# Kernel optimization log

Hardware: AMD Instinct MI355X
Metric: run time of the kernel (lower is better)

## Reference

```python
import jax, jax.numpy as jnp
import numpy as np

B, N, C = 8, 1024, 768
H = 12
HD = C // H
FF = 2048
NUM_CLASSES = 1000
SCALE = HD ** -0.5


def layer_norm(x, g, b, eps=1e-5):
    mu = jnp.mean(x, axis=-1, keepdims=True)
    var = jnp.var(x, axis=-1, keepdims=True)
    return (x - mu) * jax.lax.rsqrt(var + eps) * g + b


def setup_inputs() -> dict:
    key = jax.random.key(0)
    ks = jax.random.split(key, 12)
    s = lambda *sh: 0.02
    return {
        "src": jax.random.normal(ks[0], (B, N, C), jnp.float32),
        "y": jax.random.uniform(ks[1], (B, NUM_CLASSES), jnp.float32),
        "scorenet_h_src": jax.random.normal(ks[2], (B, NUM_CLASSES), jnp.float32),
        "pre_g": jnp.ones((C,), jnp.float32),
        "pre_b": jnp.zeros((C,), jnp.float32),
        "qkv_w": jax.random.normal(ks[3], (C, 3 * C), jnp.float32) * 0.02,
        "proj_w": jax.random.normal(ks[4], (C, C), jnp.float32) * 0.02,
        "proj_b": jnp.zeros((C,), jnp.float32),
        "n1_g": jnp.ones((C,), jnp.float32),
        "n1_b": jnp.zeros((C,), jnp.float32),
        "l1_w": jax.random.normal(ks[5], (C, FF), jnp.float32) * 0.02,
        "l1_b": jnp.zeros((FF,), jnp.float32),
        "l2_w": jax.random.normal(ks[6], (FF, C), jnp.float32) * 0.02,
        "l2_b": jnp.zeros((C,), jnp.float32),
    }


def attention(x, qkv_w, proj_w, proj_b):
    # x: [B, N, C] -> qkv: [B, N, 3, H, HD]
    qkv = (x @ qkv_w).reshape(B, N, 3, H, HD)
    qkv = jnp.transpose(qkv, (2, 0, 3, 1, 4))  # [3, B, H, N, HD]
    q, k, v = qkv[0], qkv[1], qkv[2]
    attn = jax.nn.softmax(jnp.einsum("bhqd,bhkd->bhqk", q, k) * SCALE, axis=-1)
    out = jnp.einsum("bhqk,bhkd->bhqd", attn, v)  # [B, H, N, HD]
    out = jnp.transpose(out, (0, 2, 1, 3)).reshape(B, N, C)
    out = out @ proj_w + proj_b
    return out, attn


def reference(src, y, scorenet_h_src, pre_g, pre_b, qkv_w, proj_w, proj_b,
              n1_g, n1_b, l1_w, l1_b, l2_w, l2_b):
    # eval-mode forward: dropout / drop_path are identity, mixup branches off
    x, attn = attention(layer_norm(src, pre_g, pre_b), qkv_w, proj_w, proj_b)
    src = src + x
    src_n = layer_norm(src, n1_g, n1_b)
    ffn = jax.nn.gelu(src_n @ l1_w + l1_b, approximate=False) @ l2_w + l2_b
    src = src_n + ffn
    return (src, scorenet_h_src, y, attn)
```

## Files before the change

### kernel.cpp

```cpp
#include <hip/hip_runtime.h>
#include <stdint.h>

typedef unsigned short u16;
typedef __bf16 bf16x8 __attribute__((ext_vector_type(8)));
typedef float f32x4 __attribute__((ext_vector_type(4)));


__device__ __forceinline__ u16 f2bf(float f) {
  union { float f; unsigned u; } v; v.f = f;
  unsigned r = v.u + 0x7fffu + ((v.u >> 16) & 1u);
  return (u16)(r >> 16);
}
__device__ __forceinline__ float bf2f(unsigned u) {
  union { unsigned u; float f; } v; v.u = u << 16; return v.f;
}

__device__ __forceinline__ void async16(const void* g, void* l) {
  __builtin_amdgcn_global_load_lds(
      (const __attribute__((address_space(1))) void*)g,
      (__attribute__((address_space(3))) void*)l, 16, 0, 0);
}

__device__ __forceinline__ f32x4 mfma16(bf16x8 a, bf16x8 b, f32x4 c) {
  return __builtin_amdgcn_mfma_f32_16x16x32_bf16(a, b, c, 0, 0, 0);
}

__device__ __forceinline__ float gelu_exact(float x) {
  return 0.5f * x * (1.0f + erff(x * 0.70710678118654752440f));
}

#define VMCNT(n) asm volatile("s_waitcnt vmcnt(" #n ")" ::: "memory")
#define LGKM0 asm volatile("s_waitcnt lgkmcnt(0)" ::: "memory")
#define SCHED0 __builtin_amdgcn_sched_barrier(0)
#define BAR __builtin_amdgcn_s_barrier()

__global__ __launch_bounds__(256) void ln_kernel(
    const float* __restrict__ x, const float* __restrict__ g,
    const float* __restrict__ b, u16* __restrict__ obf,
    float* __restrict__ of) {
  const size_t row = blockIdx.x;
  const float* xr = x + row * 768;
  const int t = threadIdx.x;
  const int w = t >> 6, lane = t & 63;
  float v0 = xr[t], v1 = xr[t + 256], v2 = xr[t + 512];
  float s = v0 + v1 + v2;
  float sq = v0 * v0 + v1 * v1 + v2 * v2;
#pragma unroll
  for (int off = 32; off > 0; off >>= 1) {
    s += __shfl_down(s, off);
    sq += __shfl_down(sq, off);
  }
  __shared__ float ss[4], ssq[4];
  if (lane == 0) { ss[w] = s; ssq[w] = sq; }
  __syncthreads();
  s = ss[0] + ss[1] + ss[2] + ss[3];
  sq = ssq[0] + ssq[1] + ssq[2] + ssq[3];
  const float mean = s * (1.0f / 768.0f);
  const float var = sq * (1.0f / 768.0f) - mean * mean;
  const float rstd = rsqrtf(var + 1e-5f);
  float y0 = (v0 - mean) * rstd * g[t] + b[t];
  float y1 = (v1 - mean) * rstd * g[t + 256] + b[t + 256];
  float y2 = (v2 - mean) * rstd * g[t + 512] + b[t + 512];
  obf[row * 768 + t] = f2bf(y0);
  obf[row * 768 + t + 256] = f2bf(y1);
  obf[row * 768 + t + 512] = f2bf(y2);
  if (of) {
    of[row * 768 + t] = y0;
    of[row * 768 + t + 256] = y1;
    of[row * 768 + t + 512] = y2;
  }
}

__device__ __forceinline__ void transpose_tile(float (*tile)[33],
                                               const float* __restrict__ W,
                                               u16* __restrict__ Wt, int K,
                                               int N, int bx, int by) {
  const int n0 = bx * 32, k0 = by * 32;
  const int tx = threadIdx.x, ty = threadIdx.y;
  for (int r = ty; r < 32; r += 8)
    tile[r][tx] = W[(size_t)(k0 + r) * N + n0 + tx];
  __syncthreads();
  for (int r = ty; r < 32; r += 8)
    Wt[(size_t)(n0 + r) * K + k0 + tx] = f2bf(tile[tx][r]);
}

__global__ void misc_kernel(const float* __restrict__ qkv_w,
                            const float* __restrict__ proj_w,
                            const float* __restrict__ l1_w,
                            const float* __restrict__ l2_w,
                            u16* __restrict__ qkvwT, u16* __restrict__ projwT,
                            u16* __restrict__ l1wT, u16* __restrict__ l2wT,
                            const float* __restrict__ y,
                            const float* __restrict__ sc,
                            float* __restrict__ out) {
  __shared__ float tile[32][33];
  int bid = blockIdx.x;
  if (bid < 1728) { transpose_tile(tile, qkv_w, qkvwT, 768, 2304, bid % 72, bid / 72); return; }
  bid -= 1728;
  if (bid < 576) { transpose_tile(tile, proj_w, projwT, 768, 768, bid % 24, bid / 24); return; }
  bid -= 576;
  if (bid < 1536) { transpose_tile(tile, l1_w, l1wT, 768, 2048, bid % 64, bid / 64); return; }
  bid -= 1536;
  if (bid < 1536) { transpose_tile(tile, l2_w, l2wT, 2048, 768, bid % 24, bid / 24); return; }
  bid -= 1536;
  const int t = threadIdx.y * 32 + threadIdx.x;
  const int i = bid * 256 + t;
  if (i < 8000) {
    out[6291456 + i] = sc[i];
    out[6299456 + i] = y[i];
  }
}

__global__ void vt_kernel(const u16* __restrict__ qkv, u16* __restrict__ vt) {
  const int bh = blockIdx.z, b = bh / 12, h = bh % 12;
  const int n0 = blockIdx.x * 32, d0 = blockIdx.y * 32;
  __shared__ u16 tile[32][33];
  const u16* Vp = qkv + (size_t)b * 1024 * 2304 + 1536 + h * 64;
  const int tx = threadIdx.x, ty = threadIdx.y;
  for (int r = ty; r < 32; r += 8)
    tile[r][tx] = Vp[(size_t)(n0 + r) * 2304 + d0 + tx];
  __syncthreads();
  u16* Op = vt + (size_t)bh * 64 * 1024;
  for (int r = ty; r < 32; r += 8)
    Op[(size_t)(d0 + r) * 1024 + n0 + tx] = tile[tx][r];
}

template <int BM, int BN, int GN, int WM, int WN>
__global__ __launch_bounds__(256) void gemm_kernel(
    const u16* __restrict__ A, int lda, const u16* __restrict__ Bt, int ldb,
    const float* __restrict__ bias, const float* __restrict__ res,
    float* __restrict__ outF, u16* __restrict__ outB, int ldc, int K,
    int act) {
  __shared__ u16 As[2][BM * 32];
  __shared__ u16 Bs[2][BN * 32];
  const int tid = threadIdx.x;
  const int w = tid >> 6, lane = tid & 63;
  const size_t mBase = (size_t)blockIdx.y * BM;
  const size_t nBase = (size_t)blockIdx.x * BN;
  const int rq = lane >> 2;
  const int k8 = (lane & 3) * 8;
  const int wmBase = (w / GN) * (WM * 16);
  const int wnBase = (w % GN) * (WN * 16);
  const int tm = lane & 15, kq = lane >> 4;
  const f32x4 zero = {0.f, 0.f, 0.f, 0.f};
  f32x4 acc[WM][WN];
#pragma unroll
  for (int i = 0; i < WM; i++)
#pragma unroll
    for (int j = 0; j < WN; j++) acc[i][j] = zero;

#pragma unroll
  for (int c = w; c < BM / 16; c += 4)
    async16(A + (mBase + c * 16 + rq) * lda + k8, &As[0][c * 16 * 32]);
#pragma unroll
  for (int c = w; c < BN / 16; c += 4)
    async16(Bt + (nBase + c * 16 + rq) * ldb + k8, &Bs[0][c * 16 * 32]);

  int cur = 0;
  for (int kt = 0; kt < K; kt += 32) {
    __syncthreads();
    if (kt + 32 < K) {
      const int nxt = cur ^ 1;
#pragma unroll
      for (int c = w; c < BM / 16; c += 4)
        async16(A + (mBase + c * 16 + rq) * lda + kt + 32 + k8,
                &As[nxt][c * 16 * 32]);
#pragma unroll
      for (int c = w; c < BN / 16; c += 4)
        async16(Bt + (nBase + c * 16 + rq) * ldb + kt + 32 + k8,
                &Bs[nxt][c * 16 * 32]);
    }
    bf16x8 af[WM], bfv[WN];
#pragma unroll
    for (int i = 0; i < WM; i++)
      af[i] = *(const bf16x8*)&As[cur][(wmBase + i * 16 + tm) * 32 + kq * 8];
#pragma unroll
    for (int j = 0; j < WN; j++)
      bfv[j] = *(const bf16x8*)&Bs[cur][(wnBase + j * 16 + tm) * 32 + kq * 8];
#pragma unroll
    for (int i = 0; i < WM; i++)
#pragma unroll
      for (int j = 0; j < WN; j++) acc[i][j] = mfma16(af[i], bfv[j], acc[i][j]);
    cur ^= 1;
  }

#pragma unroll
  for (int i = 0; i < WM; i++) {
    const size_t row0 = mBase + wmBase + i * 16 + kq * 4;
#pragma unroll
    for (int j = 0; j < WN; j++) {
      const size_t col = nBase + wnBase + j * 16 + tm;
      const float bv = bias ? bias[col] : 0.0f;
#pragma unroll
      for (int r = 0; r < 4; r++) {
        const size_t rr = row0 + r;
        float v = acc[i][j][r] + bv;
        if (act) v = gelu_exact(v);
        if (res) v += res[rr * ldc + col];
        if (outF) outF[rr * ldc + col] = v;
        if (outB) outB[rr * ldc + col] = f2bf(v);
      }
    }
  }
}

#define QUAD(P)                                                              \
  __builtin_amdgcn_s_setprio(1);                                             \
  _Pragma("unroll") for (int i2 = 0; i2 < 2; ++i2) {                         \
    _Pragma("unroll") for (int j = 0; j < 4; ++j) {                          \
      acc[(P)*2 + i2][j] = mfma16(aF[i2][0], bF[j][0], acc[(P)*2 + i2][j]);  \
      acc[(P)*2 + i2][j] = mfma16(aF[i2][1], bF[j][1], acc[(P)*2 + i2][j]);  \
    }                                                                        \
  }                                                                          \
  __builtin_amdgcn_s_setprio(0);

template <int ACT>
__global__ __launch_bounds__(512, 2) void gemm256_kernel(
    const u16* __restrict__ A, int lda, const u16* __restrict__ Bt, int ldb,
    const float* __restrict__ bias, u16* __restrict__ outB, int ldc, int K,
    int NX, int nwg8) {
  __shared__ u16 As[2][256 * 64];
  __shared__ u16 Bs[2][256 * 64];
  const int tid = threadIdx.x;
  const int w = tid >> 6, lane = tid & 63;
  const int wr = w >> 2, wc = w & 3;
  const int tm = lane & 15, kq = lane >> 4;
  const int id = blockIdx.x;
  const int wg = (id & 7) * nwg8 + (id >> 3);
  const size_t mBase = (size_t)(wg / NX) * 256;
  const size_t nBase = (size_t)(wg % NX) * 256;
  const int srow = tid >> 3;
  const int gch = (tid & 7) ^ (srow & 7);

#define STAGE_B(buf, kt, rb)                                          \
  async16(Bt + (nBase + (rb) + srow) * (size_t)ldb + (kt) + gch * 8,  \
          &Bs[buf][(rb) * 64 + tid * 8])
#define STAGE_A(buf, kt, rb)                                          \
  async16(A + (mBase + (rb) + srow) * (size_t)lda + (kt) + gch * 8,   \
          &As[buf][(rb) * 64 + tid * 8])

  f32x4 acc[8][4];
  const f32x4 zero = {0.f, 0.f, 0.f, 0.f};
#pragma unroll
  for (int i = 0; i < 8; ++i)
#pragma unroll
    for (int j = 0; j < 4; ++j) acc[i][j] = zero;

  auto rdA = [&](int buf, int i, int s) -> bf16x8 {
    const int rl = wr * 128 + i * 16 + tm;
    const int ch = (s * 4 + kq) ^ (rl & 7);
    return *(const bf16x8*)&As[buf][rl * 64 + ch * 8];
  };
  auto rdB = [&](int buf, int j, int s) -> bf16x8 {
    const int rl = wc * 64 + j * 16 + tm;
    const int ch = (s * 4 + kq) ^ (rl & 7);
    return *(const bf16x8*)&Bs[buf][rl * 64 + ch * 8];
  };

  STAGE_B(0, 0, 0); STAGE_B(0, 0, 64); STAGE_B(0, 0, 128); STAGE_B(0, 0, 192);
  STAGE_A(0, 0, 0); STAGE_A(0, 0, 128); STAGE_A(0, 0, 64); STAGE_A(0, 0, 192);
  VMCNT(2);
  BAR;

  const int T = K >> 6;
  bf16x8 bF[4][2], aF[2][2];
  for (int t = 0; t < T; ++t) {
    const int cur = t & 1, nxt = cur ^ 1;
    const int kt1 = (t + 1) << 6;
    const bool last = (t == T - 1);
#pragma unroll
    for (int j = 0; j < 4; ++j) { bF[j][0] = rdB(cur, j, 0); bF[j][1] = rdB(cur, j, 1); }
    aF[0][0] = rdA(cur, 0, 0); aF[0][1] = rdA(cur, 0, 1);
    aF[1][0] = rdA(cur, 1, 0); aF[1][1] = rdA(cur, 1, 1);
    if (!last) { STAGE_B(nxt, kt1, 0); STAGE_B(nxt, kt1, 64); }
    BAR; LGKM0; SCHED0;
    QUAD(0);
    BAR;
    aF[0][0] = rdA(cur, 2, 0); aF[0][1] = rdA(cur, 2, 1);
    aF[1][0] = rdA(cur, 3, 0); aF[1][1] = rdA(cur, 3, 1);
    if (!last) { STAGE_B(nxt, kt1, 128); STAGE_B(nxt, kt1, 192); VMCNT(4); }
    else { VMCNT(0); }
    BAR; LGKM0; SCHED0;
    QUAD(1);
    BAR;
    aF[0][0] = rdA(cur, 4, 0); aF[0][1] = rdA(cur, 4, 1);
    aF[1][0] = rdA(cur, 5, 0); aF[1][1] = rdA(cur, 5, 1);
    if (!last) { STAGE_A(nxt, kt1, 0); STAGE_A(nxt, kt1, 128); }
    BAR; LGKM0; SCHED0;
    QUAD(2);
    BAR;
    aF[0][0] = rdA(cur, 6, 0); aF[0][1] = rdA(cur, 6, 1);
    aF[1][0] = rdA(cur, 7, 0); aF[1][1] = rdA(cur, 7, 1);
    if (!last) { STAGE_A(nxt, kt1, 64); STAGE_A(nxt, kt1, 192); VMCNT(2); }
    BAR; LGKM0; SCHED0;
    QUAD(3);
    BAR;
  }

#pragma unroll
  for (int i = 0; i < 8; ++i) {
    const size_t row0 = mBase + wr * 128 + i * 16 + kq * 4;
#pragma unroll
    for (int j = 0; j < 4; ++j) {
      const size_t col = nBase + wc * 64 + j * 16 + tm;
      const float bv = bias ? bias[col] : 0.0f;
#pragma unroll
      for (int r = 0; r < 4; ++r) {
        float v = acc[i][j][r] + bv;
        if (ACT) v = gelu_exact(v);
        outB[(row0 + r) * ldc + col] = f2bf(v);
      }
    }
  }
#undef STAGE_A
#undef STAGE_B
}

__global__ __launch_bounds__(256, 3) void flash_kernel(
    const u16* __restrict__ qkv, const u16* __restrict__ vt,
    float* __restrict__ attn, u16* __restrict__ aout) {
  __shared__ u16 Qs[32 * 64];
  __shared__ u16 KV[2 * 128 * 64];
  __shared__ u16 Ps[32 * 128];
  __shared__ float psum[4][32];
  __shared__ float rinv[32];
  const int tid = threadIdx.x;
  const int w = tid >> 6, lane = tid & 63;
  const int tm = lane & 15, kq = lane >> 4;
  const int bh = blockIdx.y, b = bh / 12, h = bh % 12;
  const size_t m0 = (size_t)blockIdx.x * 32;
  const u16* Qp = qkv + (size_t)b * 1024 * 2304 + h * 64;
  const u16* Kp = Qp + 768;
  const u16* Vp = vt + (size_t)bh * 64 * 1024;
  float* Ab = attn + ((size_t)bh * 1024 + m0) * 1024;

  {
    const int r = tid >> 3, c = tid & 7;
    *(uint4*)&Qs[r * 64 + ((c ^ (r & 7)) * 8)] =
        *(const uint4*)(Qp + (m0 + r) * 2304 + c * 8);
  }
  __syncthreads();
  bf16x8 aq[2][2];
#pragma unroll
  for (int i = 0; i < 2; i++)
#pragma unroll
    for (int k2 = 0; k2 < 2; k2++) {
      const int m = i * 16 + tm;
      aq[i][k2] =
          *(const bf16x8*)&Qs[m * 64 + (((k2 * 4 + kq) ^ (m & 7)) * 8)];
    }

  f32x4 rs[2] = {{0.f, 0.f, 0.f, 0.f}, {0.f, 0.f, 0.f, 0.f}};
  for (int cc = 0; cc < 4; ++cc) {
    const int nc = cc * 256;
    __syncthreads();
#pragma unroll
    for (int u = 0; u < 8; ++u) {
      const int idx = u * 256 + tid;
      const int r = idx >> 3, c = idx & 7;
      *(uint4*)&KV[r * 64 + ((c ^ (r & 7)) * 8)] =
          *(const uint4*)(Kp + (size_t)(nc + r) * 2304 + c * 8);
    }
    __syncthreads();
#pragma unroll
    for (int jj = 0; jj < 4; ++jj) {
      const int n = (w * 4 + jj) * 16 + tm;
      bf16x8 bk[2];
#pragma unroll
      for (int k2 = 0; k2 < 2; k2++)
        bk[k2] =
            *(const bf16x8*)&KV[n * 64 + (((k2 * 4 + kq) ^ (n & 7)) * 8)];
#pragma unroll
      for (int i = 0; i < 2; i++) {
        f32x4 s = {0.f, 0.f, 0.f, 0.f};
        s = mfma16(aq[i][0], bk[0], s);
        s = mfma16(aq[i][1], bk[1], s);
#pragma unroll
        for (int r = 0; r < 4; r++) rs[i][r] += __expf(s[r] * 0.125f);
      }
    }
  }
#pragma unroll
  for (int i = 0; i < 2; i++)
#pragma unroll
    for (int r = 0; r < 4; r++) {
      float v = rs[i][r];
      v += __shfl_xor(v, 1); v += __shfl_xor(v, 2);
      v += __shfl_xor(v, 4); v += __shfl_xor(v, 8);
      if (tm == 0) psum[w][i * 16 + kq * 4 + r] = v;
    }
  __syncthreads();
  if (tid < 32)
    rinv[tid] =
        1.0f / (psum[0][tid] + psum[1][tid] + psum[2][tid] + psum[3][tid]);

  const f32x4 zero = {0.f, 0.f, 0.f, 0.f};
  f32x4 oacc[2] = {zero, zero};
  const int mi = w & 1, dp = w >> 1;
  for (int cc = 0; cc < 8; ++cc) {
    const int nc = cc * 128;
    __syncthreads();
#pragma unroll
    for (int u = 0; u < 4; ++u) {
      const int idx = u * 256 + tid;
      const int r = idx >> 3, c = idx & 7;
      *(uint4*)&KV[r * 64 + ((c ^ (r & 7)) * 8)] =
          *(const uint4*)(Kp + (size_t)(nc + r) * 2304 + c * 8);
    }
#pragma unroll
    for (int u = 0; u < 4; ++u) {
      const int idx = u * 256 + tid;
      const int d = idx >> 4, c = idx & 15;
      *(uint4*)&KV[8192 + d * 128 + ((c ^ (d & 15)) * 8)] =
          *(const uint4*)(Vp + (size_t)d * 1024 + nc + c * 8);
    }
    __syncthreads();
#pragma unroll
    for (int jj = 0; jj < 2; ++jj) {
      const int nb = w * 2 + jj;
      const int n = nb * 16 + tm;
      bf16x8 bk[2];
#pragma unroll
      for (int k2 = 0; k2 < 2; k2++)
        bk[k2] =
            *(const bf16x8*)&KV[n * 64 + (((k2 * 4 + kq) ^ (n & 7)) * 8)];
#pragma unroll
      for (int i = 0; i < 2; i++) {
        f32x4 s = {0.f, 0.f, 0.f, 0.f};
        s = mfma16(aq[i][0], bk[0], s);
        s = mfma16(aq[i][1], bk[1], s);
        const int row = i * 16 + kq * 4;
#pragma unroll
        for (int r = 0; r < 4; r++) {
          const float p = __expf(s[r] * 0.125f) * rinv[row + r];
          Ab[(size_t)(row + r) * 1024 + nc + nb * 16 + tm] = p;
          const int pr = row + r, pn = nb * 16 + tm;
          Ps[pr * 128 + (((pn >> 3) ^ (pr & 7)) * 8) + (pn & 7)] = f2bf(p);
        }
      }
    }
    __syncthreads();
#pragma unroll
    for (int k2 = 0; k2 < 4; ++k2) {
      const int m = mi * 16 + tm;
      const bf16x8 ap =
          *(const bf16x8*)&Ps[m * 128 + (((k2 * 4 + kq) ^ (m & 7)) * 8)];
#pragma unroll
      for (int jd = 0; jd < 2; ++jd) {
        const int d = dp * 32 + jd * 16 + tm;
        const bf16x8 bv = *(const bf16x8*)&KV[8192 + d * 128 +
                                              (((k2 * 4 + kq) ^ (d & 15)) * 8)];
        oacc[jd] = mfma16(ap, bv, oacc[jd]);
      }
    }
  }
#pragma unroll
  for (int jd = 0; jd < 2; ++jd)
#pragma unroll
    for (int r = 0; r < 4; ++r) {
      const size_t gm = (size_t)b * 1024 + m0 + mi * 16 + kq * 4 + r;
      aout[gm * 768 + h * 64 + dp * 32 + jd * 16 + tm] = f2bf(oacc[jd][r]);
    }
}

extern "C" void kernel_launch(void* const* d_in, const int* in_sizes, int n_in,
                              void* d_out, int out_size, void* d_ws,
                              size_t ws_size, hipStream_t stream) {
  const float* src    = (const float*)d_in[0];
  const float* yin    = (const float*)d_in[1];
  const float* scin   = (const float*)d_in[2];
  const float* pre_g  = (const float*)d_in[3];
  const float* pre_b  = (const float*)d_in[4];
  const float* qkv_w  = (const float*)d_in[5];
  const float* proj_w = (const float*)d_in[6];
  const float* proj_b = (const float*)d_in[7];
  const float* n1_g   = (const float*)d_in[8];
  const float* n1_b   = (const float*)d_in[9];
  const float* l1_w   = (const float*)d_in[10];
  const float* l1_b   = (const float*)d_in[11];
  const float* l2_w   = (const float*)d_in[12];
  const float* l2_b   = (const float*)d_in[13];
  float* outp = (float*)d_out;
  float* attn = outp + 6307456;

  char* ws = (char*)d_ws;
  u16* qkvwT  = (u16*)(ws + 0ull);
  u16* projwT = (u16*)(ws + 3538944ull);
  u16* l1wT   = (u16*)(ws + 4718592ull);
  u16* l2wT   = (u16*)(ws + 7864320ull);
  const size_t P0 = 11010048ull;
  u16* xn   = (u16*)(ws + P0);
  u16* qkv  = (u16*)(ws + P0 + 12582912ull);
  u16* vt   = (u16*)(ws + P0 + 50331648ull);
  u16* aout = (u16*)(ws + P0 + 62914560ull);
  float* src2 = (float*)(ws + P0);
  u16*  snb   = (u16*)(ws + P0 + 25165824ull);
  u16*  hbuf  = (u16*)(ws + P0 + 37748736ull);
  float* snf  = (float*)(ws + P0 + 71303168ull);

  dim3 tb(32, 8);
  misc_kernel<<<5439, tb, 0, stream>>>(qkv_w, proj_w, l1_w, l2_w, qkvwT,
                                       projwT, l1wT, l2wT, yin, scin, outp);
  ln_kernel<<<8192, 256, 0, stream>>>(src, pre_g, pre_b, xn, nullptr);
  gemm256_kernel<0><<<288, 512, 0, stream>>>(xn, 768, qkvwT, 768, nullptr,
                                             qkv, 2304, 768, 9, 36);
  vt_kernel<<<dim3(32, 2, 96), tb, 0, stream>>>(qkv, vt);
  flash_kernel<<<dim3(32, 96), 256, 0, stream>>>(qkv, vt, attn, aout);
  gemm_kernel<64, 128, 4, 4, 2><<<dim3(6, 128), 256, 0, stream>>>(
      aout, 768, projwT, 768, proj_b, src, src2, nullptr, 768, 768, 0);
  ln_kernel<<<8192, 256, 0, stream>>>(src2, n1_g, n1_b, snb, snf);
  gemm256_kernel<1><<<256, 512, 0, stream>>>(snb, 768, l1wT, 768, l1_b,
                                             hbuf, 2048, 768, 8, 32);
  gemm_kernel<64, 128, 4, 4, 2><<<dim3(6, 128), 256, 0, stream>>>(
      hbuf, 2048, l2wT, 2048, l2_b, snf, outp, nullptr, 768, 2048, 0);
}
```

Before: 807.1 us.

## Use 256x256 pipelined GEMM for proj/FFN2 and vectorize attention-prob stores

Replaces the simple 64x128 GEMM used for the projection and second FFN layer with the tuned 256x256 gemm256 kernel. That kernel gains residual-add and fp32-output epilogue support. In the flash kernel, each lane's four probability values are transposed across lanes with shuffles so the fp32 attention matrix is written with float4 stores instead of scalar stores. The larger tiles give only 96 workgroups for the two N=768 GEMMs, which can leave many CUs idle.

```diff
diff --git a/kernel.cpp b/kernel.cpp
--- a/kernel.cpp
+++ b/kernel.cpp
@@ -125,85 +125,6 @@
     Op[(size_t)(d0 + r) * 1024 + n0 + tx] = tile[tx][r];
 }
 
-template <int BM, int BN, int GN, int WM, int WN>
-__global__ __launch_bounds__(256) void gemm_kernel(
-    const u16* __restrict__ A, int lda, const u16* __restrict__ Bt, int ldb,
-    const float* __restrict__ bias, const float* __restrict__ res,
-    float* __restrict__ outF, u16* __restrict__ outB, int ldc, int K,
-    int act) {
-  __shared__ u16 As[2][BM * 32];
-  __shared__ u16 Bs[2][BN * 32];
-  const int tid = threadIdx.x;
-  const int w = tid >> 6, lane = tid & 63;
-  const size_t mBase = (size_t)blockIdx.y * BM;
-  const size_t nBase = (size_t)blockIdx.x * BN;
-  const int rq = lane >> 2;
-  const int k8 = (lane & 3) * 8;
-  const int wmBase = (w / GN) * (WM * 16);
-  const int wnBase = (w % GN) * (WN * 16);
-  const int tm = lane & 15, kq = lane >> 4;
-  const f32x4 zero = {0.f, 0.f, 0.f, 0.f};
-  f32x4 acc[WM][WN];
-#pragma unroll
-  for (int i = 0; i < WM; i++)
-#pragma unroll
-    for (int j = 0; j < WN; j++) acc[i][j] = zero;
-
-#pragma unroll
-  for (int c = w; c < BM / 16; c += 4)
-    async16(A + (mBase + c * 16 + rq) * lda + k8, &As[0][c * 16 * 32]);
-#pragma unroll
-  for (int c = w; c < BN / 16; c += 4)
-    async16(Bt + (nBase + c * 16 + rq) * ldb + k8, &Bs[0][c * 16 * 32]);
-
-  int cur = 0;
-  for (int kt = 0; kt < K; kt += 32) {
-    __syncthreads();
-    if (kt + 32 < K) {
-      const int nxt = cur ^ 1;
-#pragma unroll
-      for (int c = w; c < BM / 16; c += 4)
-        async16(A + (mBase + c * 16 + rq) * lda + kt + 32 + k8,
-                &As[nxt][c * 16 * 32]);
-#pragma unroll
-      for (int c = w; c < BN / 16; c += 4)
-        async16(Bt + (nBase + c * 16 + rq) * ldb + kt + 32 + k8,
-                &Bs[nxt][c * 16 * 32]);
-    }
-    bf16x8 af[WM], bfv[WN];
-#pragma unroll
-    for (int i = 0; i < WM; i++)
-      af[i] = *(const bf16x8*)&As[cur][(wmBase + i * 16 + tm) * 32 + kq * 8];
-#pragma unroll
-    for (int j = 0; j < WN; j++)
-      bfv[j] = *(const bf16x8*)&Bs[cur][(wnBase + j * 16 + tm) * 32 + kq * 8];
-#pragma unroll
-    for (int i = 0; i < WM; i++)
-#pragma unroll
-      for (int j = 0; j < WN; j++) acc[i][j] = mfma16(af[i], bfv[j], acc[i][j]);
-    cur ^= 1;
-  }
-
-#pragma unroll
-  for (int i = 0; i < WM; i++) {
-    const size_t row0 = mBase + wmBase + i * 16 + kq * 4;
-#pragma unroll
-    for (int j = 0; j < WN; j++) {
-      const size_t col = nBase + wnBase + j * 16 + tm;
-      const float bv = bias ? bias[col] : 0.0f;
-#pragma unroll
-      for (int r = 0; r < 4; r++) {
-        const size_t rr = row0 + r;
-        float v = acc[i][j][r] + bv;
-        if (act) v = gelu_exact(v);
-        if (res) v += res[rr * ldc + col];
-        if (outF) outF[rr * ldc + col] = v;
-        if (outB) outB[rr * ldc + col] = f2bf(v);
-      }
-    }
-  }
-}
-
 #define QUAD(P)                                                              \
   __builtin_amdgcn_s_setprio(1);                                             \
   _Pragma("unroll") for (int i2 = 0; i2 < 2; ++i2) {                         \
@@ -217,7 +138,8 @@
 template <int ACT>
 __global__ __launch_bounds__(512, 2) void gemm256_kernel(
     const u16* __restrict__ A, int lda, const u16* __restrict__ Bt, int ldb,
-    const float* __restrict__ bias, u16* __restrict__ outB, int ldc, int K,
+    const float* __restrict__ bias, const float* __restrict__ res,
+    float* __restrict__ outF, u16* __restrict__ outB, int ldc, int K,
     int NX, int nwg8) {
   __shared__ u16 As[2][256 * 64];
   __shared__ u16 Bs[2][256 * 64];
@@ -306,9 +228,12 @@
       const float bv = bias ? bias[col] : 0.0f;
 #pragma unroll
       for (int r = 0; r < 4; ++r) {
+        const size_t rr = row0 + r;
         float v = acc[i][j][r] + bv;
         if (ACT) v = gelu_exact(v);
-        outB[(row0 + r) * ldc + col] = f2bf(v);
+        if (res) v += res[rr * ldc + col];
+        if (outF) outF[rr * ldc + col] = v;
+        if (outB) outB[rr * ldc + col] = f2bf(v);
       }
     }
   }
@@ -430,13 +355,26 @@
         s = mfma16(aq[i][0], bk[0], s);
         s = mfma16(aq[i][1], bk[1], s);
         const int row = i * 16 + kq * 4;
+        f32x4 pv;
 #pragma unroll
         for (int r = 0; r < 4; r++) {
           const float p = __expf(s[r] * 0.125f) * rinv[row + r];
-          Ab[(size_t)(row + r) * 1024 + nc + nb * 16 + tm] = p;
+          pv[r] = p;
           const int pr = row + r, pn = nb * 16 + tm;
           Ps[pr * 128 + (((pn >> 3) ^ (pr & 7)) * 8) + (pn & 7)] = f2bf(p);
         }
+        float a0 = pv[0], a1 = pv[1], a2 = pv[2], a3 = pv[3];
+        float sx = (lane & 1) ? a0 : a1;
+        float sy = (lane & 1) ? a2 : a3;
+        sx = __shfl_xor(sx, 1); sy = __shfl_xor(sy, 1);
+        if (lane & 1) { a0 = sx; a2 = sy; } else { a1 = sx; a3 = sy; }
+        float tx = (lane & 2) ? a0 : a2;
+        float ty = (lane & 2) ? a1 : a3;
+        tx = __shfl_xor(tx, 2); ty = __shfl_xor(ty, 2);
+        if (lane & 2) { a0 = tx; a1 = ty; } else { a2 = tx; a3 = ty; }
+        float4 st = {a0, a1, a2, a3};
+        *(float4*)&Ab[(size_t)(i * 16 + kq * 4 + (tm & 3)) * 1024 + nc +
+                      nb * 16 + (tm >> 2) * 4] = st;
       }
     }
     __syncthreads();
@@ -503,14 +441,18 @@
                                        projwT, l1wT, l2wT, yin, scin, outp);
   ln_kernel<<<8192, 256, 0, stream>>>(src, pre_g, pre_b, xn, nullptr);
   gemm256_kernel<0><<<288, 512, 0, stream>>>(xn, 768, qkvwT, 768, nullptr,
-                                             qkv, 2304, 768, 9, 36);
+                                             nullptr, nullptr, qkv, 2304, 768,
+                                             9, 36);
   vt_kernel<<<dim3(32, 2, 96), tb, 0, stream>>>(qkv, vt);
   flash_kernel<<<dim3(32, 96), 256, 0, stream>>>(qkv, vt, attn, aout);
-  gemm_kernel<64, 128, 4, 4, 2><<<dim3(6, 128), 256, 0, stream>>>(
-      aout, 768, projwT, 768, proj_b, src, src2, nullptr, 768, 768, 0);
+  gemm256_kernel<0><<<96, 512, 0, stream>>>(aout, 768, projwT, 768, proj_b,
+                                            src, src2, nullptr, 768, 768,
+                                            3, 12);
   ln_kernel<<<8192, 256, 0, stream>>>(src2, n1_g, n1_b, snb, snf);
   gemm256_kernel<1><<<256, 512, 0, stream>>>(snb, 768, l1wT, 768, l1_b,
-                                             hbuf, 2048, 768, 8, 32);
-  gemm_kernel<64, 128, 4, 4, 2><<<dim3(6, 128), 256, 0, stream>>>(
-      hbuf, 2048, l2wT, 2048, l2_b, snf, outp, nullptr, 768, 2048, 0);
-}
+                                             nullptr, nullptr, hbuf, 2048, 768,
+                                             8, 32);
+  gemm256_kernel<0><<<96, 512, 0, stream>>>(hbuf, 2048, l2wT, 2048, l2_b,
+                                            snf, outp, nullptr, 768, 2048,
+                                            3, 12);
+}
```

After: 907.3 us. +12.4%, slower.
